# Kernel optimization log

Hardware: AMD Instinct MI355X
Metric: run time of the kernel (lower is better)

The kernel has to match this reference:

```python
import jax, jax.numpy as jnp
import numpy as np

B, S, H = 4, 2048, 1024
NH, HD = 16, 64
WIN = 64  # window_size = min(64, seq_len)
SCALE = float(np.sqrt(HD))


def setup_inputs() -> dict:
    key = jax.random.key(0)
    ks = jax.random.split(key, 10)
    w = lambda k, shp: (jax.random.normal(k, shp, jnp.float32) * 0.02)
    return {
        "x": jax.random.normal(ks[0], (B, S, H), jnp.float32),
        "attention_mask": jnp.ones((B, S), jnp.int32),
        "Wq": w(ks[1], (H, NH * HD)), "bq": jnp.zeros((NH * HD,), jnp.float32),
        "Wk": w(ks[2], (H, NH * HD)), "bk": jnp.zeros((NH * HD,), jnp.float32),
        "Wv": w(ks[3], (H, NH * HD)), "bv": jnp.zeros((NH * HD,), jnp.float32),
        "Wo": w(ks[4], (NH * HD, H)), "bo": jnp.zeros((H,), jnp.float32),
    }


def reference(x, attention_mask, Wq, bq, Wk, bk, Wv, bv, Wo, bo):
    # projections -> [B, NH, S, HD]
    def split_heads(t):
        return t.reshape(B, S, NH, HD).transpose(0, 2, 1, 3)
    q = split_heads(x @ Wq + bq)
    k = split_heads(x @ Wk + bk)
    v = split_heads(x @ Wv + bv)

    scores = jnp.einsum("bhqd,bhkd->bhqk", q, k) / SCALE  # [B,NH,S,S]

    # local banded mask: |i - j| <= window_size // 2
    idx = jnp.arange(S)
    local = jnp.abs(idx[None, :] - idx[:, None]) <= (WIN // 2)  # [S,S]
    scores = jnp.where(local[None, None, :, :], scores, -jnp.inf)

    # padding mask: [B,1,1,S]
    scores = jnp.where(attention_mask[:, None, None, :] == 0, -jnp.inf, scores)

    probs = jax.nn.softmax(scores, axis=-1)
    probs = jnp.nan_to_num(probs)  # rows that are fully masked -> 0

    out = jnp.einsum("bhqk,bhkd->bhqd", probs, v)
    out = out.transpose(0, 2, 1, 3).reshape(B, S, NH * HD)
    return out @ Wo + bo
```

## Files before the change

### kernel.cpp

```cpp
#include <hip/hip_runtime.h>
#include <stdint.h>

typedef unsigned short u16;
typedef __attribute__((ext_vector_type(8))) short short8;
typedef __attribute__((ext_vector_type(4))) float f32x4;

#define S_LEN 2048
#define HID   1024
#define QKV_LD 3072
#define M_ROWS 8192

__device__ __forceinline__ u16 f2bf(float f) {
  unsigned u = __float_as_uint(f);
  unsigned r = (u + 0x7fffu + ((u >> 16) & 1u)) >> 16;
  return (u16)r;
}

__device__ __forceinline__ void gload16(const u16* g, u16* l) {
  __builtin_amdgcn_global_load_lds(
      (const __attribute__((address_space(1))) unsigned int*)(g),
      (__attribute__((address_space(3))) unsigned int*)(l),
      16, 0, 0);
}

__device__ __forceinline__ void wgbar() {
  asm volatile("" ::: "memory");
  __builtin_amdgcn_s_barrier();
  asm volatile("" ::: "memory");
}

__global__ __launch_bounds__(256) void prep(
    const float* __restrict__ x, u16* __restrict__ xb,
    const float* __restrict__ bq, const float* __restrict__ bk,
    const float* __restrict__ bv, float* __restrict__ bqkv,
    const float* __restrict__ Wq, const float* __restrict__ Wk,
    const float* __restrict__ Wv, const float* __restrict__ Wo,
    u16* __restrict__ wqkvt, u16* __restrict__ wot) {
  __shared__ float tile[32][33];
  const int bid = blockIdx.x;
  if (bid < 4096) {
    int i = (bid * 256 + threadIdx.x) * 8;
    float4 a = *(const float4*)(x + i);
    float4 b = *(const float4*)(x + i + 4);
    u16 t[8];
    t[0] = f2bf(a.x); t[1] = f2bf(a.y); t[2] = f2bf(a.z); t[3] = f2bf(a.w);
    t[4] = f2bf(b.x); t[5] = f2bf(b.y); t[6] = f2bf(b.z); t[7] = f2bf(b.w);
    *(short8*)(xb + i) = *(short8*)t;
    return;
  }
  if (bid == 4096) {
    for (int i = threadIdx.x; i < 3072; i += 256)
      bqkv[i] = (i < 1024) ? bq[i] : (i < 2048) ? bk[i - 1024] : bv[i - 2048];
    return;
  }
  const int wid = bid - 4097;
  const int z = wid >> 10, rem = wid & 1023;
  const float* in = (z == 0) ? Wq : (z == 1) ? Wk : (z == 2) ? Wv : Wo;
  u16* out = (z < 3) ? (wqkvt + (size_t)z * 1024 * 1024) : wot;
  int tx = threadIdx.x & 31, ty = threadIdx.x >> 5;
  int n0 = (rem & 31) * 32, k0 = (rem >> 5) * 32;
#pragma unroll
  for (int i = 0; i < 32; i += 8)
    tile[ty + i][tx] = in[(size_t)(k0 + ty + i) * 1024 + n0 + tx];
  __syncthreads();
#pragma unroll
  for (int i = 0; i < 32; i += 8)
    out[(size_t)(n0 + ty + i) * 1024 + k0 + tx] = f2bf(tile[tx][ty + i]);
}

__global__ __launch_bounds__(256, 2) void gemm_k1(
    const u16* __restrict__ A, const u16* __restrict__ Bt,
    const float* __restrict__ bias, u16* __restrict__ C) {
  constexpr int K = 1024, NT = 16, N = 3072;
  constexpr int AU = 128 * 64;
  constexpr int SLAB = 320 * 64;
  __shared__ __align__(16) u16 smem[2 * SLAB];

  const int tid = threadIdx.x;
  const int wave = tid >> 6, lane = tid & 63;
  const int qlane = lane & 15, kgrp = lane >> 4;
  const int wm = wave >> 1, wn = wave & 1;
  int wg = blockIdx.x;
  wg = (wg & 7) * 128 + (wg >> 3);
  const int bm = wg >> 4, bn = wg & 15;

  const int srow = tid >> 3;
  const int sslot = (tid & 7) ^ (srow & 7);
  uint32_t gA[4], gB[6];
#pragma unroll
  for (int u = 0; u < 4; ++u)
    gA[u] = (uint32_t)((bm * 128 + u * 32 + srow) * K + sslot * 8);
#pragma unroll
  for (int u = 0; u < 6; ++u)
    gB[u] = (uint32_t)((bn * 192 + u * 32 + srow) * K + sslot * 8);

  auto stgA = [&](int t, int u) {
    gload16(A + (size_t)gA[u] + t * 64, &smem[(t & 1) * SLAB + u * 2048 + tid * 8]);
  };
  auto stgB = [&](int t, int u) {
    gload16(Bt + (size_t)gB[u] + t * 64, &smem[(t & 1) * SLAB + AU + u * 2048 + tid * 8]);
  };

  int aaddr[4], baddr[6];
#pragma unroll
  for (int mf = 0; mf < 4; ++mf) {
    int r = wm * 64 + mf * 16 + qlane;
    aaddr[mf] = r * 64;
  }
#pragma unroll
  for (int nf = 0; nf < 6; ++nf) {
    int r = wn * 96 + nf * 16 + qlane;
    baddr[nf] = AU + r * 64;
  }
  const int arow7 = (wm * 64 + qlane) & 7;
  const int brow7 = (wn * 96 + qlane) & 7;

  f32x4 acc[4][6] = {};
  short8 af[4][2], bf[4][2];

#pragma unroll
  for (int u = 0; u < 4; ++u) stgA(0, u);
#pragma unroll
  for (int u = 0; u < 6; ++u) stgB(0, u);
#pragma unroll
  for (int u = 0; u < 4; ++u) stgA(1, u);
  stgB(1, 0); stgB(1, 1); stgB(1, 3); stgB(1, 4);
  asm volatile("s_waitcnt vmcnt(8)" ::: "memory");
  wgbar();

  for (int t = 0; t < NT; ++t) {
    const u16* bp = &smem[(t & 1) * SLAB];

#pragma unroll
    for (int mf = 0; mf < 4; ++mf)
#pragma unroll
      for (int kk = 0; kk < 2; ++kk)
        af[mf][kk] = *(const short8*)&bp[aaddr[mf] + (((kk * 4 + kgrp) ^ arow7) * 8)];
#pragma unroll
    for (int nf = 0; nf < 4; ++nf)
#pragma unroll
      for (int kk = 0; kk < 2; ++kk)
        bf[nf][kk] = *(const short8*)&bp[baddr[nf] + (((kk * 4 + kgrp) ^ brow7) * 8)];
    if (t + 1 < NT) { stgB(t + 1, 2); stgB(t + 1, 5); }
    wgbar();
    asm volatile("s_waitcnt lgkmcnt(0)" ::: "memory");
    __builtin_amdgcn_s_setprio(1);
#pragma unroll
    for (int mf = 0; mf < 4; ++mf)
#pragma unroll
      for (int nf = 0; nf < 4; ++nf)
#pragma unroll
        for (int kk = 0; kk < 2; ++kk)
          acc[mf][nf] = __builtin_amdgcn_mfma_f32_16x16x32_bf16(
              af[mf][kk], bf[nf][kk], acc[mf][nf], 0, 0, 0);
    __builtin_amdgcn_s_setprio(0);
    wgbar();

#pragma unroll
    for (int nf = 0; nf < 2; ++nf)
#pragma unroll
      for (int kk = 0; kk < 2; ++kk)
        bf[nf][kk] = *(const short8*)&bp[baddr[nf + 4] + (((kk * 4 + kgrp) ^ brow7) * 8)];
    if (t + 2 < NT) {
      stgA(t + 2, 0); stgA(t + 2, 1); stgA(t + 2, 2); stgA(t + 2, 3);
      stgB(t + 2, 0); stgB(t + 2, 1); stgB(t + 2, 3); stgB(t + 2, 4);
    }
    wgbar();
    asm volatile("s_waitcnt lgkmcnt(0)" ::: "memory");
    __builtin_amdgcn_s_setprio(1);
#pragma unroll
    for (int mf = 0; mf < 4; ++mf)
#pragma unroll
      for (int nf = 0; nf < 2; ++nf)
#pragma unroll
        for (int kk = 0; kk < 2; ++kk)
          acc[mf][nf + 4] = __builtin_amdgcn_mfma_f32_16x16x32_bf16(
              af[mf][kk], bf[nf][kk], acc[mf][nf + 4], 0, 0, 0);
    __builtin_amdgcn_s_setprio(0);
    if (t + 2 < NT)      asm volatile("s_waitcnt vmcnt(8)" ::: "memory");
    else if (t + 1 < NT) asm volatile("s_waitcnt vmcnt(0)" ::: "memory");
    if (t + 1 < NT) wgbar();
  }

#pragma unroll
  for (int nf = 0; nf < 6; ++nf) {
    int col = bn * 192 + wn * 96 + nf * 16 + qlane;
    float bv = bias[col];
#pragma unroll
    for (int mf = 0; mf < 4; ++mf) {
      int row0 = bm * 128 + wm * 64 + mf * 16 + kgrp * 4;
#pragma unroll
      for (int r = 0; r < 4; ++r)
        C[(size_t)(row0 + r) * N + col] = f2bf(acc[mf][nf][r] + bv);
    }
  }
}

__global__ __launch_bounds__(256, 2) void gemm_k2(
    const u16* __restrict__ A, const u16* __restrict__ Bt,
    const float* __restrict__ bias, float* __restrict__ C) {
  constexpr int K = 1024, NT = 16, N = 1024;
  constexpr int AU = 128 * 64;
  constexpr int SLAB = 256 * 64;
  __shared__ __align__(16) u16 smem[2 * SLAB];

  const int tid = threadIdx.x;
  const int wave = tid >> 6, lane = tid & 63;
  const int qlane = lane & 15, kgrp = lane >> 4;
  const int wm = wave >> 1, wn = wave & 1;
  int wg = blockIdx.x;
  wg = (wg & 7) * 64 + (wg >> 3);
  const int bm = wg >> 3, bn = wg & 7;

  const int srow = tid >> 3;
  const int sslot = (tid & 7) ^ (srow & 7);
  uint32_t gA[4], gB[4];
#pragma unroll
  for (int u = 0; u < 4; ++u) {
    gA[u] = (uint32_t)((bm * 128 + u * 32 + srow) * K + sslot * 8);
    gB[u] = (uint32_t)((bn * 128 + u * 32 + srow) * K + sslot * 8);
  }
  auto stgA = [&](int t, int u) {
    gload16(A + (size_t)gA[u] + t * 64, &smem[(t & 1) * SLAB + u * 2048 + tid * 8]);
  };
  auto stgB = [&](int t, int u) {
    gload16(Bt + (size_t)gB[u] + t * 64, &smem[(t & 1) * SLAB + AU + u * 2048 + tid * 8]);
  };

  int aaddr[4], baddr[4];
#pragma unroll
  for (int f = 0; f < 4; ++f) {
    aaddr[f] = (wm * 64 + f * 16 + qlane) * 64;
    baddr[f] = AU + (wn * 64 + f * 16 + qlane) * 64;
  }
  const int arow7 = (wm * 64 + qlane) & 7;
  const int brow7 = (wn * 64 + qlane) & 7;

  f32x4 acc[4][4] = {};
  short8 af[4][2], bf[2][2];

#pragma unroll
  for (int u = 0; u < 4; ++u) stgA(0, u);
#pragma unroll
  for (int u = 0; u < 4; ++u) stgB(0, u);
#pragma unroll
  for (int u = 0; u < 4; ++u) stgA(1, u);
  stgB(1, 0); stgB(1, 2);
  asm volatile("s_waitcnt vmcnt(6)" ::: "memory");
  wgbar();

  for (int t = 0; t < NT; ++t) {
    const u16* bp = &smem[(t & 1) * SLAB];

#pragma unroll
    for (int mf = 0; mf < 4; ++mf)
#pragma unroll
      for (int kk = 0; kk < 2; ++kk)
        af[mf][kk] = *(const short8*)&bp[aaddr[mf] + (((kk * 4 + kgrp) ^ arow7) * 8)];
#pragma unroll
    for (int nf = 0; nf < 2; ++nf)
#pragma unroll
      for (int kk = 0; kk < 2; ++kk)
        bf[nf][kk] = *(const short8*)&bp[baddr[nf] + (((kk * 4 + kgrp) ^ brow7) * 8)];
    if (t + 1 < NT) { stgB(t + 1, 1); stgB(t + 1, 3); }
    wgbar();
    asm volatile("s_waitcnt lgkmcnt(0)" ::: "memory");
    __builtin_amdgcn_s_setprio(1);
#pragma unroll
    for (int mf = 0; mf < 4; ++mf)
#pragma unroll
      for (int nf = 0; nf < 2; ++nf)
#pragma unroll
        for (int kk = 0; kk < 2; ++kk)
          acc[mf][nf] = __builtin_amdgcn_mfma_f32_16x16x32_bf16(
              af[mf][kk], bf[nf][kk], acc[mf][nf], 0, 0, 0);
    __builtin_amdgcn_s_setprio(0);
    wgbar();

#pragma unroll
    for (int nf = 0; nf < 2; ++nf)
#pragma unroll
      for (int kk = 0; kk < 2; ++kk)
        bf[nf][kk] = *(const short8*)&bp[baddr[nf + 2] + (((kk * 4 + kgrp) ^ brow7) * 8)];
    if (t + 2 < NT) {
      stgA(t + 2, 0); stgA(t + 2, 1); stgA(t + 2, 2); stgA(t + 2, 3);
      stgB(t + 2, 0); stgB(t + 2, 2);
    }
    wgbar();
    asm volatile("s_waitcnt lgkmcnt(0)" ::: "memory");
    __builtin_amdgcn_s_setprio(1);
#pragma unroll
    for (int mf = 0; mf < 4; ++mf)
#pragma unroll
      for (int nf = 0; nf < 2; ++nf)
#pragma unroll
        for (int kk = 0; kk < 2; ++kk)
          acc[mf][nf + 2] = __builtin_amdgcn_mfma_f32_16x16x32_bf16(
              af[mf][kk], bf[nf][kk], acc[mf][nf + 2], 0, 0, 0);
    __builtin_amdgcn_s_setprio(0);
    if (t + 2 < NT)      asm volatile("s_waitcnt vmcnt(6)" ::: "memory");
    else if (t + 1 < NT) asm volatile("s_waitcnt vmcnt(0)" ::: "memory");
    if (t + 1 < NT) wgbar();
  }

#pragma unroll
  for (int nf = 0; nf < 4; ++nf) {
    int col = bn * 128 + wn * 64 + nf * 16 + qlane;
    float bv = bias[col];
#pragma unroll
    for (int mf = 0; mf < 4; ++mf) {
      int row0 = bm * 128 + wm * 64 + mf * 16 + kgrp * 4;
#pragma unroll
      for (int r = 0; r < 4; ++r)
        C[(size_t)(row0 + r) * N + col] = acc[mf][nf][r] + bv;
    }
  }
}

__global__ __launch_bounds__(256, 2) void attn_local(
    const u16* __restrict__ qkv, const int* __restrict__ amask,
    u16* __restrict__ aout) {
  __shared__ __align__(16) u16 Kl[192][72];
  __shared__ __align__(16) u16 Vt[64][200];
  __shared__ __align__(16) u16 Pl[4][32][104];

  const int tid = threadIdx.x, wave = tid >> 6, lane = tid & 63;
  const int qlane = lane & 15, kgrp = lane >> 4;
  const int bz = blockIdx.x;
  const int qt = bz & 15, h = (bz >> 4) & 15, b = bz >> 8;
  const int qs0 = qt * 128;
  const int jt = qs0 - 32;
  const size_t rbase = (size_t)b * S_LEN;

  {
    const int r0 = tid >> 3, c0 = (tid & 7) * 8;
#pragma unroll
    for (int p = 0; p < 6; ++p) {
      int row = p * 32 + r0;
      int j = jt + row;
      u16 kv[8], vv[8];
      if (j >= 0 && j < S_LEN) {
        const u16* kp = qkv + (rbase + j) * QKV_LD + HID + h * 64 + c0;
        *(short8*)kv = *(const short8*)kp;
        *(short8*)vv = *(const short8*)(kp + HID);
      } else {
#pragma unroll
        for (int q = 0; q < 8; ++q) { kv[q] = 0; vv[q] = 0; }
      }
      *(short8*)&Kl[row][c0] = *(short8*)kv;
#pragma unroll
      for (int q = 0; q < 8; ++q) Vt[c0 + q][row] = vv[q];
    }
  }

  short8 qf[2][2];
#pragma unroll
  for (int mf = 0; mf < 2; ++mf)
#pragma unroll
    for (int kk = 0; kk < 2; ++kk)
      qf[mf][kk] = *(const short8*)(qkv +
          (rbase + qs0 + wave * 32 + mf * 16 + qlane) * QKV_LD +
          h * 64 + kk * 32 + kgrp * 8);

  __syncthreads();

  f32x4 sc[2][6] = {};
#pragma unroll
  for (int kk = 0; kk < 2; ++kk) {
    short8 kf[6];
#pragma unroll
    for (int nf = 0; nf < 6; ++nf)
      kf[nf] = *(const short8*)&Kl[wave * 32 + nf * 16 + qlane][kk * 32 + kgrp * 8];
#pragma unroll
    for (int mf = 0; mf < 2; ++mf)
#pragma unroll
      for (int nf = 0; nf < 6; ++nf)
        sc[mf][nf] = __builtin_amdgcn_mfma_f32_16x16x32_bf16(
            qf[mf][kk], kf[nf], sc[mf][nf], 0, 0, 0);
  }

  int jcol[6], mv[6];
#pragma unroll
  for (int nf = 0; nf < 6; ++nf) {
    int j = jt + wave * 32 + nf * 16 + qlane;
    jcol[nf] = j;
    mv[nf] = (j >= 0 && j < S_LEN) ? amask[rbase + j] : 0;
  }

  float inv[2][4];
#pragma unroll
  for (int mf = 0; mf < 2; ++mf) {
    const int irow0 = qs0 + wave * 32 + mf * 16 + kgrp * 4;
    float mx[4] = {-1e30f, -1e30f, -1e30f, -1e30f};
#pragma unroll
    for (int r = 0; r < 4; ++r) {
      int i = irow0 + r;
#pragma unroll
      for (int nf = 0; nf < 6; ++nf) {
        int d = i - jcol[nf];
        if (mv[nf] && d >= -32 && d <= 32) mx[r] = fmaxf(mx[r], sc[mf][nf][r]);
      }
    }
#pragma unroll
    for (int m = 1; m < 16; m <<= 1)
#pragma unroll
      for (int r = 0; r < 4; ++r)
        mx[r] = fmaxf(mx[r], __shfl_xor(mx[r], m));
    float sm[4] = {0.f, 0.f, 0.f, 0.f};
#pragma unroll
    for (int r = 0; r < 4; ++r) {
      int i = irow0 + r;
#pragma unroll
      for (int nf = 0; nf < 6; ++nf) {
        int d = i - jcol[nf];
        bool val = mv[nf] && d >= -32 && d <= 32;
        float p = val ? __expf((sc[mf][nf][r] - mx[r]) * 0.125f) : 0.f;
        sc[mf][nf][r] = p;
        sm[r] += p;
      }
    }
#pragma unroll
    for (int m = 1; m < 16; m <<= 1)
#pragma unroll
      for (int r = 0; r < 4; ++r)
        sm[r] += __shfl_xor(sm[r], m);
#pragma unroll
    for (int r = 0; r < 4; ++r)
      inv[mf][r] = sm[r] > 0.f ? 1.f / sm[r] : 0.f;
#pragma unroll
    for (int nf = 0; nf < 6; ++nf)
#pragma unroll
      for (int r = 0; r < 4; ++r)
        Pl[wave][mf * 16 + kgrp * 4 + r][nf * 16 + qlane] = f2bf(sc[mf][nf][r]);
  }
  __syncthreads();

  f32x4 oc[2][4] = {};
#pragma unroll
  for (int ks = 0; ks < 3; ++ks) {
    short8 pa[2], vb[4];
#pragma unroll
    for (int mf = 0; mf < 2; ++mf)
      pa[mf] = *(const short8*)&Pl[wave][mf * 16 + qlane][ks * 32 + kgrp * 8];
#pragma unroll
    for (int nf = 0; nf < 4; ++nf)
      vb[nf] = *(const short8*)&Vt[nf * 16 + qlane][wave * 32 + ks * 32 + kgrp * 8];
#pragma unroll
    for (int mf = 0; mf < 2; ++mf)
#pragma unroll
      for (int nf = 0; nf < 4; ++nf)
        oc[mf][nf] = __builtin_amdgcn_mfma_f32_16x16x32_bf16(
            pa[mf], vb[nf], oc[mf][nf], 0, 0, 0);
  }

#pragma unroll
  for (int mf = 0; mf < 2; ++mf)
#pragma unroll
    for (int nf = 0; nf < 4; ++nf)
#pragma unroll
      for (int r = 0; r < 4; ++r) {
        size_t row = rbase + qs0 + wave * 32 + mf * 16 + kgrp * 4 + r;
        aout[row * HID + h * 64 + nf * 16 + qlane] =
            f2bf(oc[mf][nf][r] * inv[mf][r]);
      }
}

extern "C" void kernel_launch(void* const* d_in, const int* in_sizes, int n_in,
                              void* d_out, int out_size, void* d_ws, size_t ws_size,
                              hipStream_t stream) {
  const float* x  = (const float*)d_in[0];
  const int* amask = (const int*)d_in[1];
  const float* Wq = (const float*)d_in[2];
  const float* bq = (const float*)d_in[3];
  const float* Wk = (const float*)d_in[4];
  const float* bk = (const float*)d_in[5];
  const float* Wv = (const float*)d_in[6];
  const float* bv = (const float*)d_in[7];
  const float* Wo = (const float*)d_in[8];
  const float* bo = (const float*)d_in[9];
  float* out = (float*)d_out;

  char* w = (char*)d_ws;
  u16* xb    = (u16*)w;   w += (size_t)M_ROWS * HID * 2;
  u16* wqkvt = (u16*)w;   w += (size_t)3072 * 1024 * 2;
  u16* wot   = (u16*)w;   w += (size_t)1024 * 1024 * 2;
  float* bqkv = (float*)w; w += 3072 * 4 + 256;
  u16* qkv   = (u16*)w;   w += (size_t)M_ROWS * 3072 * 2;
  u16* aout  = (u16*)w;   w += (size_t)M_ROWS * HID * 2;

  prep<<<8193, 256, 0, stream>>>(x, xb, bq, bk, bv, bqkv,
                                 Wq, Wk, Wv, Wo, wqkvt, wot);
  gemm_k1<<<1024, 256, 0, stream>>>(xb, wqkvt, bqkv, qkv);
  attn_local<<<1024, 256, 0, stream>>>(qkv, amask, aout);
  gemm_k2<<<512, 256, 0, stream>>>(aout, wot, bo, out);
}
```

Baseline: 115.3 us.

## Enlarge QKV GEMM tile to 256x384 with 8 waves and triple-buffered LDS

Rewrites the QKV projection GEMM to use 512-thread blocks computing 256x384 output tiles, with each wave owning a 128x96 sub-tile. The K step drops to 32 and staging moves into a three-slot LDS ring with a new paired-row swizzle. The larger per-wave tile raises MFMA work per LDS load, and the three-slot ring lets the block keep two loads in flight with a single barrier per step. The cost is 192 accumulator registers per thread, only 256 blocks for the grid to spread over the CUs, and a tile shape that may leave some CUs idle.

Measured after the change: 128.2 us. +11.2%, slower.

```diff
diff --git a/kernel.cpp b/kernel.cpp
--- a/kernel.cpp
+++ b/kernel.cpp
@@ -68,127 +68,104 @@
     out[(size_t)(n0 + ty + i) * 1024 + k0 + tx] = f2bf(tile[tx][ty + i]);
 }
 
-__global__ __launch_bounds__(256, 2) void gemm_k1(
+__global__ __launch_bounds__(512, 2)
+__attribute__((amdgpu_waves_per_eu(2, 2)))
+void gemm_k1(
     const u16* __restrict__ A, const u16* __restrict__ Bt,
     const float* __restrict__ bias, u16* __restrict__ C) {
-  constexpr int K = 1024, NT = 16, N = 3072;
-  constexpr int AU = 128 * 64;
-  constexpr int SLAB = 320 * 64;
-  __shared__ __align__(16) u16 smem[2 * SLAB];
+  constexpr int K = 1024, NT = 32, N = 3072;
+  constexpr int SLOT = 20480;
+  constexpr int BOFF = 8192;
+  __shared__ __align__(16) u16 smem[3 * SLOT];
 
   const int tid = threadIdx.x;
   const int wave = tid >> 6, lane = tid & 63;
   const int qlane = lane & 15, kgrp = lane >> 4;
-  const int wm = wave >> 1, wn = wave & 1;
+  const int wm = wave >> 2, wn = wave & 3;
   int wg = blockIdx.x;
-  wg = (wg & 7) * 128 + (wg >> 3);
-  const int bm = wg >> 4, bn = wg & 15;
-
-  const int srow = tid >> 3;
-  const int sslot = (tid & 7) ^ (srow & 7);
-  uint32_t gA[4], gB[6];
-#pragma unroll
-  for (int u = 0; u < 4; ++u)
-    gA[u] = (uint32_t)((bm * 128 + u * 32 + srow) * K + sslot * 8);
-#pragma unroll
-  for (int u = 0; u < 6; ++u)
-    gB[u] = (uint32_t)((bn * 192 + u * 32 + srow) * K + sslot * 8);
-
-  auto stgA = [&](int t, int u) {
-    gload16(A + (size_t)gA[u] + t * 64, &smem[(t & 1) * SLAB + u * 2048 + tid * 8]);
-  };
-  auto stgB = [&](int t, int u) {
-    gload16(Bt + (size_t)gB[u] + t * 64, &smem[(t & 1) * SLAB + AU + u * 2048 + tid * 8]);
-  };
-
-  int aaddr[4], baddr[6];
-#pragma unroll
-  for (int mf = 0; mf < 4; ++mf) {
-    int r = wm * 64 + mf * 16 + qlane;
-    aaddr[mf] = r * 64;
+  wg = (wg & 7) * 32 + (wg >> 3);
+  const int bm = wg >> 3, bn = wg & 7;
+
+  const int trp = tid >> 3, tp = tid & 7;
+  uint32_t aoff[2], boff[3];
+  int ldsA[2], ldsB[3];
+#pragma unroll
+  for (int i = 0; i < 2; ++i) {
+    int rp = i * 64 + trp, l = tp ^ (rp & 7);
+    int r = rp * 2 + (l >> 2), c8 = l & 3;
+    aoff[i] = (uint32_t)((bm * 256 + r) * K + c8 * 8);
+    ldsA[i] = i * 4096 + tid * 8;
+  }
+#pragma unroll
+  for (int i = 0; i < 3; ++i) {
+    int rp = i * 64 + trp, l = tp ^ (rp & 7);
+    int r = rp * 2 + (l >> 2), c8 = l & 3;
+    boff[i] = (uint32_t)((bn * 384 + r) * K + c8 * 8);
+    ldsB[i] = BOFF + i * 4096 + tid * 8;
+  }
+
+  int aaddr[8], baddr[6];
+#pragma unroll
+  for (int mf = 0; mf < 8; ++mf) {
+    int r = wm * 128 + mf * 16 + qlane;
+    aaddr[mf] = (r >> 1) * 64 + ((((r & 1) << 2) + kgrp) ^ ((r >> 1) & 7)) * 8;
   }
 #pragma unroll
   for (int nf = 0; nf < 6; ++nf) {
     int r = wn * 96 + nf * 16 + qlane;
-    baddr[nf] = AU + r * 64;
-  }
-  const int arow7 = (wm * 64 + qlane) & 7;
-  const int brow7 = (wn * 96 + qlane) & 7;
-
-  f32x4 acc[4][6] = {};
-  short8 af[4][2], bf[4][2];
-
-#pragma unroll
-  for (int u = 0; u < 4; ++u) stgA(0, u);
-#pragma unroll
-  for (int u = 0; u < 6; ++u) stgB(0, u);
-#pragma unroll
-  for (int u = 0; u < 4; ++u) stgA(1, u);
-  stgB(1, 0); stgB(1, 1); stgB(1, 3); stgB(1, 4);
-  asm volatile("s_waitcnt vmcnt(8)" ::: "memory");
+    baddr[nf] = BOFF + (r >> 1) * 64 + ((((r & 1) << 2) + kgrp) ^ ((r >> 1) & 7)) * 8;
+  }
+
+  auto stg = [&](int t) {
+    u16* base = smem + (t % 3) * SLOT;
+#pragma unroll
+    for (int i = 0; i < 2; ++i)
+      gload16(A + aoff[i] + t * 32, base + ldsA[i]);
+#pragma unroll
+    for (int i = 0; i < 3; ++i)
+      gload16(Bt + boff[i] + t * 32, base + ldsB[i]);
+  };
+
+  f32x4 acc[8][6] = {};
+
+  stg(0);
+  stg(1);
+  asm volatile("s_waitcnt vmcnt(5)" ::: "memory");
   wgbar();
 
   for (int t = 0; t < NT; ++t) {
-    const u16* bp = &smem[(t & 1) * SLAB];
-
-#pragma unroll
-    for (int mf = 0; mf < 4; ++mf)
-#pragma unroll
-      for (int kk = 0; kk < 2; ++kk)
-        af[mf][kk] = *(const short8*)&bp[aaddr[mf] + (((kk * 4 + kgrp) ^ arow7) * 8)];
-#pragma unroll
-    for (int nf = 0; nf < 4; ++nf)
-#pragma unroll
-      for (int kk = 0; kk < 2; ++kk)
-        bf[nf][kk] = *(const short8*)&bp[baddr[nf] + (((kk * 4 + kgrp) ^ brow7) * 8)];
-    if (t + 1 < NT) { stgB(t + 1, 2); stgB(t + 1, 5); }
-    wgbar();
-    asm volatile("s_waitcnt lgkmcnt(0)" ::: "memory");
-    __builtin_amdgcn_s_setprio(1);
-#pragma unroll
-    for (int mf = 0; mf < 4; ++mf)
-#pragma unroll
-      for (int nf = 0; nf < 4; ++nf)
-#pragma unroll
-        for (int kk = 0; kk < 2; ++kk)
-          acc[mf][nf] = __builtin_amdgcn_mfma_f32_16x16x32_bf16(
-              af[mf][kk], bf[nf][kk], acc[mf][nf], 0, 0, 0);
-    __builtin_amdgcn_s_setprio(0);
-    wgbar();
-
-#pragma unroll
-    for (int nf = 0; nf < 2; ++nf)
-#pragma unroll
-      for (int kk = 0; kk < 2; ++kk)
-        bf[nf][kk] = *(const short8*)&bp[baddr[nf + 4] + (((kk * 4 + kgrp) ^ brow7) * 8)];
-    if (t + 2 < NT) {
-      stgA(t + 2, 0); stgA(t + 2, 1); stgA(t + 2, 2); stgA(t + 2, 3);
-      stgB(t + 2, 0); stgB(t + 2, 1); stgB(t + 2, 3); stgB(t + 2, 4);
-    }
-    wgbar();
-    asm volatile("s_waitcnt lgkmcnt(0)" ::: "memory");
-    __builtin_amdgcn_s_setprio(1);
-#pragma unroll
-    for (int mf = 0; mf < 4; ++mf)
-#pragma unroll
-      for (int nf = 0; nf < 2; ++nf)
-#pragma unroll
-        for (int kk = 0; kk < 2; ++kk)
-          acc[mf][nf + 4] = __builtin_amdgcn_mfma_f32_16x16x32_bf16(
-              af[mf][kk], bf[nf][kk], acc[mf][nf + 4], 0, 0, 0);
-    __builtin_amdgcn_s_setprio(0);
-    if (t + 2 < NT)      asm volatile("s_waitcnt vmcnt(8)" ::: "memory");
+    const u16* bp = smem + (t % 3) * SLOT;
+    short8 af[8];
+#pragma unroll
+    for (int mf = 0; mf < 8; ++mf)
+      af[mf] = *(const short8*)&bp[aaddr[mf]];
+    if (t + 2 < NT) stg(t + 2);
+#pragma unroll
+    for (int np = 0; np < 3; ++np) {
+      short8 bf0 = *(const short8*)&bp[baddr[np * 2]];
+      short8 bf1 = *(const short8*)&bp[baddr[np * 2 + 1]];
+      __builtin_amdgcn_s_setprio(1);
+#pragma unroll
+      for (int mf = 0; mf < 8; ++mf) {
+        acc[mf][np * 2] = __builtin_amdgcn_mfma_f32_16x16x32_bf16(
+            af[mf], bf0, acc[mf][np * 2], 0, 0, 0);
+        acc[mf][np * 2 + 1] = __builtin_amdgcn_mfma_f32_16x16x32_bf16(
+            af[mf], bf1, acc[mf][np * 2 + 1], 0, 0, 0);
+      }
+      __builtin_amdgcn_s_setprio(0);
+    }
+    if (t + 2 < NT)      asm volatile("s_waitcnt vmcnt(5)" ::: "memory");
     else if (t + 1 < NT) asm volatile("s_waitcnt vmcnt(0)" ::: "memory");
     if (t + 1 < NT) wgbar();
   }
 
 #pragma unroll
   for (int nf = 0; nf < 6; ++nf) {
-    int col = bn * 192 + wn * 96 + nf * 16 + qlane;
+    int col = bn * 384 + wn * 96 + nf * 16 + qlane;
     float bv = bias[col];
 #pragma unroll
-    for (int mf = 0; mf < 4; ++mf) {
-      int row0 = bm * 128 + wm * 64 + mf * 16 + kgrp * 4;
+    for (int mf = 0; mf < 8; ++mf) {
+      int row0 = bm * 256 + wm * 128 + mf * 16 + kgrp * 4;
 #pragma unroll
       for (int r = 0; r < 4; ++r)
         C[(size_t)(row0 + r) * N + col] = f2bf(acc[mf][nf][r] + bv);
@@ -490,7 +467,7 @@
 
   prep<<<8193, 256, 0, stream>>>(x, xb, bq, bk, bv, bqkv,
                                  Wq, Wk, Wv, Wo, wqkvt, wot);
-  gemm_k1<<<1024, 256, 0, stream>>>(xb, wqkvt, bqkv, qkv);
+  gemm_k1<<<256, 512, 0, stream>>>(xb, wqkvt, bqkv, qkv);
   attn_local<<<1024, 256, 0, stream>>>(qkv, amask, aout);
   gemm_k2<<<512, 256, 0, stream>>>(aout, wot, bo, out);
 }
```

## Use 8 waves per block in QKV GEMM and remap attention block order

Applied to the files above, without the earlier changes.

The QKV projection GEMM goes from 4 to 8 waves per 128x192 tile, so each wave now computes a 64x48 sub-tile and each thread issues fewer async global-to-LDS loads per stage. The load schedule and vmcnt waits are rebalanced to match. The aim is more waves to hide latency and fewer registers per wave, at the cost of more LDS fragment reloads per MFMA. The attention kernel also permutes its block index so that consecutive blocks are spread across XCDs, which is intended to improve cache locality.

After: 112.5 us. 2.4% less time.

```diff
diff --git a/kernel.cpp b/kernel.cpp
--- a/kernel.cpp
+++ b/kernel.cpp
@@ -68,7 +68,7 @@
     out[(size_t)(n0 + ty + i) * 1024 + k0 + tx] = f2bf(tile[tx][ty + i]);
 }
 
-__global__ __launch_bounds__(256, 2) void gemm_k1(
+__global__ __launch_bounds__(512, 2) void gemm_k1(
     const u16* __restrict__ A, const u16* __restrict__ Bt,
     const float* __restrict__ bias, u16* __restrict__ C) {
   constexpr int K = 1024, NT = 16, N = 3072;
@@ -79,53 +79,44 @@
   const int tid = threadIdx.x;
   const int wave = tid >> 6, lane = tid & 63;
   const int qlane = lane & 15, kgrp = lane >> 4;
-  const int wm = wave >> 1, wn = wave & 1;
+  const int wm = wave >> 2, wn = wave & 3;
   int wg = blockIdx.x;
   wg = (wg & 7) * 128 + (wg >> 3);
   const int bm = wg >> 4, bn = wg & 15;
 
   const int srow = tid >> 3;
   const int sslot = (tid & 7) ^ (srow & 7);
-  uint32_t gA[4], gB[6];
-#pragma unroll
-  for (int u = 0; u < 4; ++u)
-    gA[u] = (uint32_t)((bm * 128 + u * 32 + srow) * K + sslot * 8);
-#pragma unroll
-  for (int u = 0; u < 6; ++u)
-    gB[u] = (uint32_t)((bn * 192 + u * 32 + srow) * K + sslot * 8);
+  uint32_t gA[2], gB[3];
+#pragma unroll
+  for (int u = 0; u < 2; ++u)
+    gA[u] = (uint32_t)((bm * 128 + u * 64 + srow) * K + sslot * 8);
+#pragma unroll
+  for (int u = 0; u < 3; ++u)
+    gB[u] = (uint32_t)((bn * 192 + u * 64 + srow) * K + sslot * 8);
 
   auto stgA = [&](int t, int u) {
-    gload16(A + (size_t)gA[u] + t * 64, &smem[(t & 1) * SLAB + u * 2048 + tid * 8]);
+    gload16(A + (size_t)gA[u] + t * 64, &smem[(t & 1) * SLAB + u * 4096 + tid * 8]);
   };
   auto stgB = [&](int t, int u) {
-    gload16(Bt + (size_t)gB[u] + t * 64, &smem[(t & 1) * SLAB + AU + u * 2048 + tid * 8]);
+    gload16(Bt + (size_t)gB[u] + t * 64, &smem[(t & 1) * SLAB + AU + u * 4096 + tid * 8]);
   };
 
-  int aaddr[4], baddr[6];
-#pragma unroll
-  for (int mf = 0; mf < 4; ++mf) {
-    int r = wm * 64 + mf * 16 + qlane;
-    aaddr[mf] = r * 64;
-  }
-#pragma unroll
-  for (int nf = 0; nf < 6; ++nf) {
-    int r = wn * 96 + nf * 16 + qlane;
-    baddr[nf] = AU + r * 64;
-  }
-  const int arow7 = (wm * 64 + qlane) & 7;
-  const int brow7 = (wn * 96 + qlane) & 7;
-
-  f32x4 acc[4][6] = {};
-  short8 af[4][2], bf[4][2];
-
-#pragma unroll
-  for (int u = 0; u < 4; ++u) stgA(0, u);
-#pragma unroll
-  for (int u = 0; u < 6; ++u) stgB(0, u);
-#pragma unroll
-  for (int u = 0; u < 4; ++u) stgA(1, u);
-  stgB(1, 0); stgB(1, 1); stgB(1, 3); stgB(1, 4);
-  asm volatile("s_waitcnt vmcnt(8)" ::: "memory");
+  const int key7 = qlane & 7;
+  int aaddr[4], baddr[3];
+#pragma unroll
+  for (int mf = 0; mf < 4; ++mf)
+    aaddr[mf] = (wm * 64 + mf * 16 + qlane) * 64;
+#pragma unroll
+  for (int nf = 0; nf < 3; ++nf)
+    baddr[nf] = AU + (wn * 48 + nf * 16 + qlane) * 64;
+
+  f32x4 acc[4][3] = {};
+  short8 af[4][2], bf[2][2];
+
+  stgA(0, 0); stgA(0, 1);
+  stgB(0, 0); stgB(0, 1); stgB(0, 2);
+  stgA(1, 0); stgA(1, 1);
+  asm volatile("s_waitcnt vmcnt(2)" ::: "memory");
   wgbar();
 
   for (int t = 0; t < NT; ++t) {
@@ -135,20 +126,20 @@
     for (int mf = 0; mf < 4; ++mf)
 #pragma unroll
       for (int kk = 0; kk < 2; ++kk)
-        af[mf][kk] = *(const short8*)&bp[aaddr[mf] + (((kk * 4 + kgrp) ^ arow7) * 8)];
-#pragma unroll
-    for (int nf = 0; nf < 4; ++nf)
-#pragma unroll
-      for (int kk = 0; kk < 2; ++kk)
-        bf[nf][kk] = *(const short8*)&bp[baddr[nf] + (((kk * 4 + kgrp) ^ brow7) * 8)];
-    if (t + 1 < NT) { stgB(t + 1, 2); stgB(t + 1, 5); }
+        af[mf][kk] = *(const short8*)&bp[aaddr[mf] + (((kk * 4 + kgrp) ^ key7) * 8)];
+#pragma unroll
+    for (int nf = 0; nf < 2; ++nf)
+#pragma unroll
+      for (int kk = 0; kk < 2; ++kk)
+        bf[nf][kk] = *(const short8*)&bp[baddr[nf] + (((kk * 4 + kgrp) ^ key7) * 8)];
+    if (t + 1 < NT) { stgB(t + 1, 0); stgB(t + 1, 1); stgB(t + 1, 2); }
     wgbar();
     asm volatile("s_waitcnt lgkmcnt(0)" ::: "memory");
     __builtin_amdgcn_s_setprio(1);
 #pragma unroll
     for (int mf = 0; mf < 4; ++mf)
 #pragma unroll
-      for (int nf = 0; nf < 4; ++nf)
+      for (int nf = 0; nf < 2; ++nf)
 #pragma unroll
         for (int kk = 0; kk < 2; ++kk)
           acc[mf][nf] = __builtin_amdgcn_mfma_f32_16x16x32_bf16(
@@ -157,34 +148,27 @@
     wgbar();
 
 #pragma unroll
-    for (int nf = 0; nf < 2; ++nf)
-#pragma unroll
-      for (int kk = 0; kk < 2; ++kk)
-        bf[nf][kk] = *(const short8*)&bp[baddr[nf + 4] + (((kk * 4 + kgrp) ^ brow7) * 8)];
-    if (t + 2 < NT) {
-      stgA(t + 2, 0); stgA(t + 2, 1); stgA(t + 2, 2); stgA(t + 2, 3);
-      stgB(t + 2, 0); stgB(t + 2, 1); stgB(t + 2, 3); stgB(t + 2, 4);
-    }
+    for (int kk = 0; kk < 2; ++kk)
+      bf[0][kk] = *(const short8*)&bp[baddr[2] + (((kk * 4 + kgrp) ^ key7) * 8)];
+    if (t + 2 < NT) { stgA(t + 2, 0); stgA(t + 2, 1); }
     wgbar();
     asm volatile("s_waitcnt lgkmcnt(0)" ::: "memory");
     __builtin_amdgcn_s_setprio(1);
 #pragma unroll
     for (int mf = 0; mf < 4; ++mf)
 #pragma unroll
-      for (int nf = 0; nf < 2; ++nf)
-#pragma unroll
-        for (int kk = 0; kk < 2; ++kk)
-          acc[mf][nf + 4] = __builtin_amdgcn_mfma_f32_16x16x32_bf16(
-              af[mf][kk], bf[nf][kk], acc[mf][nf + 4], 0, 0, 0);
+      for (int kk = 0; kk < 2; ++kk)
+        acc[mf][2] = __builtin_amdgcn_mfma_f32_16x16x32_bf16(
+            af[mf][kk], bf[0][kk], acc[mf][2], 0, 0, 0);
     __builtin_amdgcn_s_setprio(0);
-    if (t + 2 < NT)      asm volatile("s_waitcnt vmcnt(8)" ::: "memory");
+    if (t + 2 < NT)      asm volatile("s_waitcnt vmcnt(2)" ::: "memory");
     else if (t + 1 < NT) asm volatile("s_waitcnt vmcnt(0)" ::: "memory");
     if (t + 1 < NT) wgbar();
   }
 
 #pragma unroll
-  for (int nf = 0; nf < 6; ++nf) {
-    int col = bn * 192 + wn * 96 + nf * 16 + qlane;
+  for (int nf = 0; nf < 3; ++nf) {
+    int col = bn * 192 + wn * 48 + nf * 16 + qlane;
     float bv = bias[col];
 #pragma unroll
     for (int mf = 0; mf < 4; ++mf) {
@@ -326,7 +310,8 @@
 
   const int tid = threadIdx.x, wave = tid >> 6, lane = tid & 63;
   const int qlane = lane & 15, kgrp = lane >> 4;
-  const int bz = blockIdx.x;
+  const int rbz = blockIdx.x;
+  const int bz = (rbz & 7) * 128 + (rbz >> 3);
   const int qt = bz & 15, h = (bz >> 4) & 15, b = bz >> 8;
   const int qs0 = qt * 128;
   const int jt = qs0 - 32;
@@ -490,7 +475,7 @@
 
   prep<<<8193, 256, 0, stream>>>(x, xb, bq, bk, bv, bqkv,
                                  Wq, Wk, Wv, Wo, wqkvt, wot);
-  gemm_k1<<<1024, 256, 0, stream>>>(xb, wqkvt, bqkv, qkv);
+  gemm_k1<<<1024, 512, 0, stream>>>(xb, wqkvt, bqkv, qkv);
   attn_local<<<1024, 256, 0, stream>>>(qkv, amask, aout);
   gemm_k2<<<512, 256, 0, stream>>>(aout, wot, bo, out);
 }
```

## Split QKV GEMM loop into three MFMA phases and remap blocks per XCD

Applied to the files above, without the earlier changes.

The QKV GEMM main loop is restructured from two compute phases into three, each covering two N-fragments. Global-to-LDS prefetch issues are redistributed across the phases, so fewer B fragments stay in registers and there is more interleaving between loads and MFMAs. Both GEMMs now use an XCD-aware block mapping that gives each XCD a contiguous 2D patch of output tiles to improve L2 reuse, and the attention kernel's block index is swizzled the same way. The extra barrier per iteration adds synchronization overhead, and the vmcnt wait counts have to match the new load ordering.

Result: faster. 110.0 us, median of 2 (-4.5%).

```diff
diff --git a/kernel.cpp b/kernel.cpp
--- a/kernel.cpp
+++ b/kernel.cpp
@@ -73,82 +73,77 @@
     const float* __restrict__ bias, u16* __restrict__ C) {
   constexpr int K = 1024, NT = 16, N = 3072;
   constexpr int AU = 128 * 64;
-  constexpr int SLAB = 320 * 64;
-  __shared__ __align__(16) u16 smem[2 * SLAB];
+  constexpr int BUF = 320 * 64;
+  __shared__ __align__(16) u16 smem[2 * BUF];
 
   const int tid = threadIdx.x;
   const int wave = tid >> 6, lane = tid & 63;
   const int qlane = lane & 15, kgrp = lane >> 4;
   const int wm = wave >> 1, wn = wave & 1;
-  int wg = blockIdx.x;
-  wg = (wg & 7) * 128 + (wg >> 3);
-  const int bm = wg >> 4, bn = wg & 15;
+  const int wg = blockIdx.x;
+  const int xcd = wg & 7, local = wg >> 3;
+  const int bm = (xcd >> 1) * 16 + (local >> 3);
+  const int bn = (xcd & 1) * 8 + (local & 7);
 
   const int srow = tid >> 3;
-  const int sslot = (tid & 7) ^ (srow & 7);
+  const int sslot = tid & 7;
   uint32_t gA[4], gB[6];
 #pragma unroll
-  for (int u = 0; u < 4; ++u)
-    gA[u] = (uint32_t)((bm * 128 + u * 32 + srow) * K + sslot * 8);
-#pragma unroll
-  for (int u = 0; u < 6; ++u)
-    gB[u] = (uint32_t)((bn * 192 + u * 32 + srow) * K + sslot * 8);
-
-  auto stgA = [&](int t, int u) {
-    gload16(A + (size_t)gA[u] + t * 64, &smem[(t & 1) * SLAB + u * 2048 + tid * 8]);
+  for (int au = 0; au < 4; ++au) {
+    int row = au * 32 + srow;
+    gA[au] = (uint32_t)((bm * 128 + row) * K + ((sslot ^ (row & 7)) * 8));
+  }
+#pragma unroll
+  for (int bu = 0; bu < 6; ++bu) {
+    int row = bu * 32 + srow;
+    gB[bu] = (uint32_t)((bn * 192 + row) * K + ((sslot ^ (row & 7)) * 8));
+  }
+
+  auto stgA = [&](int t, int au) {
+    gload16(A + (size_t)gA[au] + t * 64, &smem[(t & 1) * BUF + au * 2048 + tid * 8]);
   };
-  auto stgB = [&](int t, int u) {
-    gload16(Bt + (size_t)gB[u] + t * 64, &smem[(t & 1) * SLAB + AU + u * 2048 + tid * 8]);
+  auto stgB = [&](int t, int bu) {
+    gload16(Bt + (size_t)gB[bu] + t * 64, &smem[(t & 1) * BUF + AU + bu * 2048 + tid * 8]);
   };
 
-  int aaddr[4], baddr[6];
-#pragma unroll
-  for (int mf = 0; mf < 4; ++mf) {
-    int r = wm * 64 + mf * 16 + qlane;
-    aaddr[mf] = r * 64;
-  }
-#pragma unroll
-  for (int nf = 0; nf < 6; ++nf) {
-    int r = wn * 96 + nf * 16 + qlane;
-    baddr[nf] = AU + r * 64;
-  }
-  const int arow7 = (wm * 64 + qlane) & 7;
-  const int brow7 = (wn * 96 + qlane) & 7;
+#pragma unroll
+  for (int au = 0; au < 4; ++au) stgA(0, au);
+#pragma unroll
+  for (int bu = 0; bu < 6; ++bu) stgB(0, bu);
+#pragma unroll
+  for (int au = 0; au < 4; ++au) stgA(1, au);
+  stgB(1, 0); stgB(1, 1);
+  asm volatile("s_waitcnt vmcnt(6)" ::: "memory");
+  wgbar();
 
   f32x4 acc[4][6] = {};
-  short8 af[4][2], bf[4][2];
-
-#pragma unroll
-  for (int u = 0; u < 4; ++u) stgA(0, u);
-#pragma unroll
-  for (int u = 0; u < 6; ++u) stgB(0, u);
-#pragma unroll
-  for (int u = 0; u < 4; ++u) stgA(1, u);
-  stgB(1, 0); stgB(1, 1); stgB(1, 3); stgB(1, 4);
-  asm volatile("s_waitcnt vmcnt(8)" ::: "memory");
-  wgbar();
+  short8 af[4][2], bf[2][2];
 
   for (int t = 0; t < NT; ++t) {
-    const u16* bp = &smem[(t & 1) * SLAB];
-
-#pragma unroll
-    for (int mf = 0; mf < 4; ++mf)
-#pragma unroll
-      for (int kk = 0; kk < 2; ++kk)
-        af[mf][kk] = *(const short8*)&bp[aaddr[mf] + (((kk * 4 + kgrp) ^ arow7) * 8)];
-#pragma unroll
-    for (int nf = 0; nf < 4; ++nf)
-#pragma unroll
-      for (int kk = 0; kk < 2; ++kk)
-        bf[nf][kk] = *(const short8*)&bp[baddr[nf] + (((kk * 4 + kgrp) ^ brow7) * 8)];
-    if (t + 1 < NT) { stgB(t + 1, 2); stgB(t + 1, 5); }
+    const u16* bp = &smem[(t & 1) * BUF];
+
+#pragma unroll
+    for (int mf = 0; mf < 4; ++mf)
+#pragma unroll
+      for (int kk = 0; kk < 2; ++kk) {
+        int r = wm * 64 + mf * 16 + qlane;
+        af[mf][kk] = *(const short8*)&bp[r * 64 + ((kk * 4 + kgrp) ^ (r & 7)) * 8];
+      }
+#pragma unroll
+    for (int nf = 0; nf < 2; ++nf)
+#pragma unroll
+      for (int kk = 0; kk < 2; ++kk) {
+        int r = wn * 96 + nf * 16 + qlane;
+        bf[nf][kk] = *(const short8*)&bp[AU + r * 64 + ((kk * 4 + kgrp) ^ (r & 7)) * 8];
+      }
+    if (t + 1 < NT) { stgB(t + 1, 2); stgB(t + 1, 3); stgB(t + 1, 4); stgB(t + 1, 5); }
     wgbar();
     asm volatile("s_waitcnt lgkmcnt(0)" ::: "memory");
     __builtin_amdgcn_s_setprio(1);
 #pragma unroll
     for (int mf = 0; mf < 4; ++mf)
 #pragma unroll
-      for (int nf = 0; nf < 4; ++nf)
+      for (int nf = 0; nf < 2; ++nf)
 #pragma unroll
         for (int kk = 0; kk < 2; ++kk)
           acc[mf][nf] = __builtin_amdgcn_mfma_f32_16x16x32_bf16(
@@ -159,12 +154,33 @@
 #pragma unroll
     for (int nf = 0; nf < 2; ++nf)
 #pragma unroll
-      for (int kk = 0; kk < 2; ++kk)
-        bf[nf][kk] = *(const short8*)&bp[baddr[nf + 4] + (((kk * 4 + kgrp) ^ brow7) * 8)];
-    if (t + 2 < NT) {
-      stgA(t + 2, 0); stgA(t + 2, 1); stgA(t + 2, 2); stgA(t + 2, 3);
-      stgB(t + 2, 0); stgB(t + 2, 1); stgB(t + 2, 3); stgB(t + 2, 4);
-    }
+      for (int kk = 0; kk < 2; ++kk) {
+        int r = wn * 96 + (nf + 2) * 16 + qlane;
+        bf[nf][kk] = *(const short8*)&bp[AU + r * 64 + ((kk * 4 + kgrp) ^ (r & 7)) * 8];
+      }
+    if (t + 2 < NT) { stgA(t + 2, 0); stgA(t + 2, 1); stgA(t + 2, 2); stgA(t + 2, 3); }
+    wgbar();
+    asm volatile("s_waitcnt lgkmcnt(0)" ::: "memory");
+    __builtin_amdgcn_s_setprio(1);
+#pragma unroll
+    for (int mf = 0; mf < 4; ++mf)
+#pragma unroll
+      for (int nf = 0; nf < 2; ++nf)
+#pragma unroll
+        for (int kk = 0; kk < 2; ++kk)
+          acc[mf][nf + 2] = __builtin_amdgcn_mfma_f32_16x16x32_bf16(
+              af[mf][kk], bf[nf][kk], acc[mf][nf + 2], 0, 0, 0);
+    __builtin_amdgcn_s_setprio(0);
+    wgbar();
+
+#pragma unroll
+    for (int nf = 0; nf < 2; ++nf)
+#pragma unroll
+      for (int kk = 0; kk < 2; ++kk) {
+        int r = wn * 96 + (nf + 4) * 16 + qlane;
+        bf[nf][kk] = *(const short8*)&bp[AU + r * 64 + ((kk * 4 + kgrp) ^ (r & 7)) * 8];
+      }
+    if (t + 2 < NT) { stgB(t + 2, 0); stgB(t + 2, 1); }
     wgbar();
     asm volatile("s_waitcnt lgkmcnt(0)" ::: "memory");
     __builtin_amdgcn_s_setprio(1);
@@ -177,7 +193,7 @@
           acc[mf][nf + 4] = __builtin_amdgcn_mfma_f32_16x16x32_bf16(
               af[mf][kk], bf[nf][kk], acc[mf][nf + 4], 0, 0, 0);
     __builtin_amdgcn_s_setprio(0);
-    if (t + 2 < NT)      asm volatile("s_waitcnt vmcnt(8)" ::: "memory");
+    if (t + 2 < NT)      asm volatile("s_waitcnt vmcnt(6)" ::: "memory");
     else if (t + 1 < NT) asm volatile("s_waitcnt vmcnt(0)" ::: "memory");
     if (t + 1 < NT) wgbar();
   }
@@ -208,9 +224,10 @@
   const int wave = tid >> 6, lane = tid & 63;
   const int qlane = lane & 15, kgrp = lane >> 4;
   const int wm = wave >> 1, wn = wave & 1;
-  int wg = blockIdx.x;
-  wg = (wg & 7) * 64 + (wg >> 3);
-  const int bm = wg >> 3, bn = wg & 7;
+  const int wg = blockIdx.x;
+  const int xcd = wg & 7, local = wg >> 3;
+  const int bm = (xcd >> 1) * 16 + (local >> 2);
+  const int bn = (xcd & 1) * 4 + (local & 3);
 
   const int srow = tid >> 3;
   const int sslot = (tid & 7) ^ (srow & 7);
@@ -326,7 +343,8 @@
 
   const int tid = threadIdx.x, wave = tid >> 6, lane = tid & 63;
   const int qlane = lane & 15, kgrp = lane >> 4;
-  const int bz = blockIdx.x;
+  const int rbz = blockIdx.x;
+  const int bz = (rbz & 7) * 128 + (rbz >> 3);
   const int qt = bz & 15, h = (bz >> 4) & 15, b = bz >> 8;
   const int qs0 = qt * 128;
   const int jt = qs0 - 32;
```
